# Kernel optimization log

Hardware: AMD Instinct MI355X
Metric: run time of the kernel (lower is better)

The kernel has to match this reference:

```python
import jax, jax.numpy as jnp
import numpy as np

B, C, H, W = 4, 512, 64, 64
HC = C // 2  # hidden_channel of Correlation


def setup_inputs() -> dict:
    key = jax.random.key(0)
    ks = jax.random.split(key, 7)
    s = 0.02
    return {
        "x": jax.random.normal(ks[0], (B, C, H, W), dtype=jnp.float32),
        "Wf": jax.random.normal(ks[1], (HC, C), dtype=jnp.float32) * s,
        "bf": jnp.zeros((HC,), dtype=jnp.float32),
        "Wg": jax.random.normal(ks[2], (HC, C), dtype=jnp.float32) * s,
        "bg": jnp.zeros((HC,), dtype=jnp.float32),
        "Wh": jax.random.normal(ks[3], (C, C), dtype=jnp.float32) * s,
        "bh": jnp.zeros((C,), dtype=jnp.float32),
    }


def reference(x, Wf, bf, Wg, bg, Wh, bh):
    b, c, h, w = x.shape
    n = h * w
    xf = x.reshape(b, c, n)  # hw_flatten: [B, C, N]
    # 1x1 convs == per-pixel linear projections
    f = jnp.einsum('oc,bcn->bon', Wf, xf) + bf[None, :, None]  # [B, HC, N]
    g = jnp.einsum('oc,bcn->bon', Wg, xf) + bg[None, :, None]  # [B, HC, N]
    hproj = jnp.einsum('oc,bcn->bon', Wh, xf) + bh[None, :, None]  # [B, C, N]
    # energy = f^T g : [B, N, N]
    energy = jnp.einsum('bcn,bcm->bnm', f, g)
    correlation = jax.nn.softmax(energy, axis=-1)
    # attention = mean over query axis n of correlation -> [B, 1, N]
    attention = jnp.mean(correlation, axis=1, keepdims=True)
    # residual = h @ correlation^T : sum_k h[b,c,k] * corr[b,j,k]
    residual = jnp.einsum('bck,bjk->bcj', hproj, correlation)
    residual = residual.reshape(b, c, h, w)
    attention = attention.reshape(b, 1, h, w)
    return residual, attention
```

## Files before the change

### kernel.cpp

```cpp
#include <hip/hip_runtime.h>
#include <cmath>

#define BATCH 4
#define CH    512
#define HCH   256
#define NPIX  4096
#define L2E   1.44269504088896340736f

typedef __attribute__((ext_vector_type(8))) short bf16x8;
typedef __attribute__((ext_vector_type(4))) float f32x4;

#define MFMA16(a, b, c) __builtin_amdgcn_mfma_f32_16x16x32_bf16((a), (b), (c), 0, 0, 0)

__device__ __forceinline__ unsigned short f2bf(float f) {
    unsigned int u = __float_as_uint(f);
    return (unsigned short)((u + 0x7fffu + ((u >> 16) & 1u)) >> 16);
}
__device__ __forceinline__ ushort4 pack4(float a, float b, float c, float d) {
    ushort4 u; u.x = f2bf(a); u.y = f2bf(b); u.z = f2bf(c); u.w = f2bf(d); return u;
}
__device__ __forceinline__ void gload16(const unsigned short* g, unsigned short* l) {
    __builtin_amdgcn_global_load_lds(
        (const __attribute__((address_space(1))) unsigned int*)g,
        (__attribute__((address_space(3))) unsigned int*)l, 16, 0, 0);
}

__global__ __launch_bounds__(256) void convert_w_kernel(
    const float* __restrict__ Wf, const float* __restrict__ Wg,
    const float* __restrict__ Wh, unsigned short* __restrict__ Wc)
{
    const int idx = blockIdx.x * 256 + threadIdx.x;
    const int o  = idx >> 7;
    const int c4 = (idx & 127) * 4;
    const float* src = (o < HCH)     ? (Wf + (size_t)o * CH + c4)
                     : (o < 2 * HCH) ? (Wg + (size_t)(o - HCH) * CH + c4)
                                     : (Wh + (size_t)(o - 2 * HCH) * CH + c4);
    float4 v = *(const float4*)src;
    *(ushort4*)&Wc[(size_t)o * CH + c4] = pack4(v.x, v.y, v.z, v.w);
}

__global__ __launch_bounds__(256) void convert_x_kernel(
    const float* __restrict__ x, unsigned short* __restrict__ Xp)
{
    __shared__ unsigned short Lt[64][40];
    const int b  = blockIdx.z;
    const int cb = blockIdx.y;
    const int n0 = blockIdx.x * 64;
    const int t  = threadIdx.x;
    const int cr = t >> 4;
    const int f4 = t & 15;
    #pragma unroll
    for (int p = 0; p < 2; ++p) {
        const int c = p * 16 + cr;
        float4 v = *(const float4*)(x + ((size_t)b * CH + cb * 32 + c) * NPIX + n0 + f4 * 4);
        Lt[f4 * 4 + 0][c] = f2bf(v.x);
        Lt[f4 * 4 + 1][c] = f2bf(v.y);
        Lt[f4 * 4 + 2][c] = f2bf(v.z);
        Lt[f4 * 4 + 3][c] = f2bf(v.w);
    }
    __syncthreads();
    const int n  = t >> 2;
    const int ch = t & 3;
    uint4 u = *(const uint4*)&Lt[n][ch * 8];
    *(uint4*)&Xp[((size_t)b * 16 + cb) * (NPIX * 32) + (size_t)(n0 + n) * 32 + ch * 8] = u;
}

__global__ __launch_bounds__(256, 2) void proj_fg_kernel(
    const unsigned short* __restrict__ Wc, const unsigned short* __restrict__ Xp,
    const float* __restrict__ bf, const float* __restrict__ bg,
    unsigned short* __restrict__ F, unsigned short* __restrict__ G)
{
    const int b  = blockIdx.z;
    const int n0 = blockIdx.x * 128;
    const int o0 = blockIdx.y * 128;
    const int t  = threadIdx.x;
    const int wave = t >> 6, lane = t & 63, quad = lane >> 4, l16 = lane & 15;
    const int ow = o0 + wave * 32;

    f32x4 acc[2][8];
    #pragma unroll
    for (int ms = 0; ms < 2; ++ms)
        #pragma unroll
        for (int ns = 0; ns < 8; ++ns) acc[ms][ns] = (f32x4){0.f, 0.f, 0.f, 0.f};

    const unsigned short* xb = Xp + (size_t)b * 16 * (NPIX * 32);
    for (int st = 0; st < 16; ++st) {
        bf16x8 a0 = *(const bf16x8*)&Wc[(size_t)(ow + l16) * CH + st * 32 + quad * 8];
        bf16x8 a1 = *(const bf16x8*)&Wc[(size_t)(ow + 16 + l16) * CH + st * 32 + quad * 8];
        const unsigned short* xs = xb + (size_t)st * (NPIX * 32) + quad * 8;
        #pragma unroll
        for (int ns = 0; ns < 8; ++ns) {
            bf16x8 bb = *(const bf16x8*)(xs + (size_t)(n0 + ns * 16 + l16) * 32);
            acc[0][ns] = MFMA16(a0, bb, acc[0][ns]);
            acc[1][ns] = MFMA16(a1, bb, acc[1][ns]);
        }
    }

    const int orow = quad * 4;
    #pragma unroll
    for (int ms = 0; ms < 2; ++ms) {
        const int ob = ow + ms * 16 + orow;
        float bias[4];
        #pragma unroll
        for (int r = 0; r < 4; ++r)
            bias[r] = (o0 < HCH) ? bf[ob + r] : bg[ob + r - HCH];
        #pragma unroll
        for (int ns = 0; ns < 8; ++ns) {
            const int n = n0 + ns * 16 + l16;
            ushort4 u = pack4(acc[ms][ns][0] + bias[0], acc[ms][ns][1] + bias[1],
                              acc[ms][ns][2] + bias[2], acc[ms][ns][3] + bias[3]);
            if (o0 < HCH) {
                *(ushort4*)&F[((size_t)b * NPIX + n) * HCH + ob] = u;
            } else {
                const int og = ob - HCH;
                const int cb = og >> 5, co = og & 31;
                *(ushort4*)&G[((size_t)b * 8 + cb) * (NPIX * 32) + (size_t)n * 32 + co] = u;
            }
        }
    }
}

__global__ __launch_bounds__(256, 2) void proj_v_kernel(
    const unsigned short* __restrict__ Wc, const unsigned short* __restrict__ Xp,
    const float* __restrict__ bh, unsigned short* __restrict__ V)
{
    const int b  = blockIdx.z;
    const int c0 = blockIdx.x * 128;
    const int p0 = blockIdx.y * 128;
    const int t  = threadIdx.x;
    const int wave = t >> 6, lane = t & 63, quad = lane >> 4, l16 = lane & 15;
    const int pw = p0 + wave * 32;

    f32x4 acc[2][8];
    #pragma unroll
    for (int ms = 0; ms < 2; ++ms)
        #pragma unroll
        for (int ns = 0; ns < 8; ++ns) acc[ms][ns] = (f32x4){0.f, 0.f, 0.f, 0.f};

    const unsigned short* xb = Xp + (size_t)b * 16 * (NPIX * 32);
    for (int st = 0; st < 16; ++st) {
        const unsigned short* xs = xb + (size_t)st * (NPIX * 32) + quad * 8;
        bf16x8 a0 = *(const bf16x8*)(xs + (size_t)(pw + l16) * 32);
        bf16x8 a1 = *(const bf16x8*)(xs + (size_t)(pw + 16 + l16) * 32);
        #pragma unroll
        for (int ns = 0; ns < 8; ++ns) {
            bf16x8 bb = *(const bf16x8*)&Wc[(size_t)(2 * HCH + c0 + ns * 16 + l16) * CH + st * 32 + quad * 8];
            acc[0][ns] = MFMA16(a0, bb, acc[0][ns]);
            acc[1][ns] = MFMA16(a1, bb, acc[1][ns]);
        }
    }

    float biasv[8];
    #pragma unroll
    for (int ns = 0; ns < 8; ++ns) biasv[ns] = bh[c0 + ns * 16 + l16];

    const int kb = pw >> 5;
    const int ko0 = quad * 4;
    const int cx = (l16 & 7) << 3;
    #pragma unroll
    for (int ms = 0; ms < 2; ++ms) {
        #pragma unroll
        for (int ns = 0; ns < 8; ++ns) {
            const int c = c0 + ns * 16 + l16;
            ushort4 u = pack4(acc[ms][ns][0] + biasv[ns], acc[ms][ns][1] + biasv[ns],
                              acc[ms][ns][2] + biasv[ns], acc[ms][ns][3] + biasv[ns]);
            const int el = (c * 32 + ms * 16 + ko0) ^ cx;
            *(ushort4*)&V[((size_t)b * 128 + kb) * (CH * 32) + el] = u;
        }
    }
}

__global__ __launch_bounds__(512, 4) void score_kernel(
    const unsigned short* __restrict__ F, const unsigned short* __restrict__ G,
    unsigned short* __restrict__ P, float* __restrict__ rowl)
{
    const int blk = blockIdx.x;
    const int xcd = blk & 7;
    const int b   = xcd >> 1;
    const int kh  = xcd & 1;
    const int q0  = (blk >> 3) * 64;
    const int t    = threadIdx.x;
    const int wave = t >> 6, lane = t & 63, quad = lane >> 4, l16 = lane & 15;
    const int qh = wave >> 2, kw = wave & 3;

    bf16x8 af[2][8];
    #pragma unroll
    for (int qs = 0; qs < 2; ++qs)
        #pragma unroll
        for (int st = 0; st < 8; ++st)
            af[qs][st] = *(const bf16x8*)&F[((size_t)b * NPIX + q0 + qh * 32 + qs * 16 + l16) * HCH + st * 32 + quad * 8];

    float ls[2][4];
    #pragma unroll
    for (int qs = 0; qs < 2; ++qs)
        #pragma unroll
        for (int r = 0; r < 4; ++r) ls[qs][r] = 0.f;

    const unsigned short* Gb = G + (size_t)b * 8 * (NPIX * 32);
    unsigned short* Pb2 = P + (size_t)b * 128 * (NPIX * 32) + (size_t)(q0 + qh * 32) * 32;
    const int qx = (quad & 1) * 4;

    const int kbeg = kh * 2048, kend = kbeg + 2048;
    for (int k0 = kbeg; k0 < kend; k0 += 128) {
        const int kk = k0 + kw * 32;
        f32x4 s[2][2];
        #pragma unroll
        for (int qs = 0; qs < 2; ++qs)
            #pragma unroll
            for (int ks = 0; ks < 2; ++ks) s[qs][ks] = (f32x4){0.f, 0.f, 0.f, 0.f};
        #pragma unroll
        for (int st = 0; st < 8; ++st) {
            const unsigned short* gs = Gb + (size_t)st * (NPIX * 32) + quad * 8;
            bf16x8 b0 = *(const bf16x8*)(gs + (size_t)(kk + l16) * 32);
            bf16x8 b1 = *(const bf16x8*)(gs + (size_t)(kk + 16 + l16) * 32);
            s[0][0] = MFMA16(af[0][st], b0, s[0][0]);
            s[1][0] = MFMA16(af[1][st], b0, s[1][0]);
            s[0][1] = MFMA16(af[0][st], b1, s[0][1]);
            s[1][1] = MFMA16(af[1][st], b1, s[1][1]);
        }

        unsigned short* pw = Pb2 + (size_t)(kk >> 5) * (NPIX * 32);
        #pragma unroll
        for (int qs = 0; qs < 2; ++qs)
            #pragma unroll
            for (int ks = 0; ks < 2; ++ks)
                #pragma unroll
                for (int r = 0; r < 4; ++r) {
                    float e = exp2f(L2E * s[qs][ks][r]);
                    const int el = ((qs * 16 + quad * 4 + r) * 32 + ks * 16 + l16)
                                   ^ ((qx + r) << 3);
                    pw[el] = f2bf(e);
                    ls[qs][r] += e;
                }
    }

    #pragma unroll
    for (int d = 1; d < 16; d <<= 1)
        #pragma unroll
        for (int qs = 0; qs < 2; ++qs)
            #pragma unroll
            for (int r = 0; r < 4; ++r) ls[qs][r] += __shfl_xor(ls[qs][r], d, 64);

    if (l16 == 0) {
        #pragma unroll
        for (int qs = 0; qs < 2; ++qs)
            #pragma unroll
            for (int r = 0; r < 4; ++r)
                atomicAdd(&rowl[(size_t)b * NPIX + q0 + qh * 32 + qs * 16 + quad * 4 + r], ls[qs][r]);
    }
}

__global__ __launch_bounds__(512, 4) void pv_kernel(
    const unsigned short* __restrict__ P, const unsigned short* __restrict__ V,
    const float* __restrict__ rowl, float* __restrict__ outres)
{
    __shared__ unsigned short Pl[2][64 * 32];
    __shared__ unsigned short Vl[2][256 * 32];
    const int blk = blockIdx.x;
    const int xcd = blk & 7;
    const int b   = xcd >> 1;
    const int ch  = xcd & 1;
    const int q0  = (blk >> 3) * 64;
    const int t    = threadIdx.x;
    const int wave = t >> 6, lane = t & 63, quad = lane >> 4, l16 = lane & 15;
    const int qw = wave >> 2;
    const int cw = wave & 3;
    const int cbase = cw * 64;

    const unsigned short* Pg = P + ((size_t)b * 128 * NPIX + q0) * 32;
    const unsigned short* Vg = V + ((size_t)b * 128 * CH + ch * 256) * 32;

    const int fx  = (l16 & 7) << 4;
    const int pA0 = (((qw * 32      + l16) * 64) + quad * 16) ^ fx;
    const int pA1 = (((qw * 32 + 16 + l16) * 64) + quad * 16) ^ fx;
    const int vO0 = (((cbase +  0 + l16) * 64) + quad * 16) ^ fx;
    const int vO1 = (((cbase + 16 + l16) * 64) + quad * 16) ^ fx;
    const int vO2 = (((cbase + 32 + l16) * 64) + quad * 16) ^ fx;
    const int vO3 = (((cbase + 48 + l16) * 64) + quad * 16) ^ fx;

    f32x4 O[2][4];
    #pragma unroll
    for (int qs = 0; qs < 2; ++qs)
        #pragma unroll
        for (int ct = 0; ct < 4; ++ct) O[qs][ct] = (f32x4){0.f, 0.f, 0.f, 0.f};

    auto stage = [&](int bb, int kb) {
        const unsigned short* vg = Vg + (size_t)kb * (CH * 32) + wave * 1024;
        unsigned short* vl = &Vl[bb][wave * 1024];
        gload16(vg + lane * 8,       vl);
        gload16(vg + 512 + lane * 8, vl + 512);
        if (wave < 4) {
            const unsigned short* pg = Pg + (size_t)kb * (NPIX * 32) + wave * 512;
            gload16(pg + lane * 8, &Pl[bb][wave * 512]);
        }
    };

    stage(0, 0);
    __syncthreads();

    int buf = 0;
    for (int kb = 0; kb < 128; ++kb) {
        if (kb + 1 < 128) stage(buf ^ 1, kb + 1);

        const char* pb = (const char*)&Pl[buf][0];
        const char* vb = (const char*)&Vl[buf][0];
        bf16x8 a0 = *(const bf16x8*)(pb + pA0);
        bf16x8 a1 = *(const bf16x8*)(pb + pA1);
        bf16x8 v0 = *(const bf16x8*)(vb + vO0);
        bf16x8 v1 = *(const bf16x8*)(vb + vO1);
        bf16x8 v2 = *(const bf16x8*)(vb + vO2);
        bf16x8 v3 = *(const bf16x8*)(vb + vO3);
        O[0][0] = MFMA16(a0, v0, O[0][0]);
        O[1][0] = MFMA16(a1, v0, O[1][0]);
        O[0][1] = MFMA16(a0, v1, O[0][1]);
        O[1][1] = MFMA16(a1, v1, O[1][1]);
        O[0][2] = MFMA16(a0, v2, O[0][2]);
        O[1][2] = MFMA16(a1, v2, O[1][2]);
        O[0][3] = MFMA16(a0, v3, O[0][3]);
        O[1][3] = MFMA16(a1, v3, O[1][3]);

        __syncthreads();
        buf ^= 1;
    }

    float lr[2][4];
    #pragma unroll
    for (int qs = 0; qs < 2; ++qs)
        #pragma unroll
        for (int r = 0; r < 4; ++r)
            lr[qs][r] = 1.0f / rowl[(size_t)b * NPIX + q0 + qw * 32 + qs * 16 + quad * 4 + r];

    const int cb2 = ch * 256 + cbase;
    #pragma unroll
    for (int qs = 0; qs < 2; ++qs) {
        #pragma unroll
        for (int ct = 0; ct < 4; ++ct) {
            f32x4 o = O[qs][ct];
            o[0] *= lr[qs][0]; o[1] *= lr[qs][1]; o[2] *= lr[qs][2]; o[3] *= lr[qs][3];
            const int c = cb2 + ct * 16 + l16;
            *(f32x4*)&outres[((size_t)b * CH + c) * NPIX + q0 + qw * 32 + qs * 16 + quad * 4] = o;
        }
    }
}

__global__ __launch_bounds__(256) void colsum_kernel(
    const unsigned short* __restrict__ P, const float* __restrict__ rowl,
    float* __restrict__ attnacc)
{
    __shared__ float CS[16][32];
    const int blk = blockIdx.x;
    const int b  = blk >> 7;
    const int kb = blk & 127;
    const int t  = threadIdx.x;
    const int ko2 = t & 15;
    const int qr  = t >> 4;
    const unsigned short* Pb = P + (size_t)(b * 128 + kb) * (NPIX * 32);
    const float* rl = rowl + (size_t)b * NPIX;
    const int qx = (qr & 7) << 3;

    float a0 = 0.f, a1 = 0.f;
    for (int q = qr; q < NPIX; q += 16) {
        unsigned int u = *(const unsigned int*)(Pb + ((q * 32 + ko2 * 2) ^ qx));
        float li = 1.0f / rl[q];
        a0 += __uint_as_float(u << 16) * li;
        a1 += __uint_as_float(u & 0xFFFF0000u) * li;
    }
    CS[qr][ko2 * 2]     = a0;
    CS[qr][ko2 * 2 + 1] = a1;
    __syncthreads();
    if (t < 32) {
        float s = 0.f;
        #pragma unroll
        for (int i = 0; i < 16; ++i) s += CS[i][t];
        attnacc[(size_t)b * NPIX + kb * 32 + t] = s;
    }
}

__global__ __launch_bounds__(512, 4) void stats_kernel(
    const unsigned short* __restrict__ F, const unsigned short* __restrict__ G,
    float* __restrict__ rowl)
{
    const int blk = blockIdx.x;
    const int xcd = blk & 7;
    const int b   = xcd >> 1;
    const int kh  = xcd & 1;
    const int q0  = (blk >> 3) * 64;
    const int t    = threadIdx.x;
    const int wave = t >> 6, lane = t & 63, quad = lane >> 4, l16 = lane & 15;
    const int qh = wave >> 2, kw = wave & 3;

    bf16x8 af[2][8];
    #pragma unroll
    for (int qs = 0; qs < 2; ++qs)
        #pragma unroll
        for (int st = 0; st < 8; ++st)
            af[qs][st] = *(const bf16x8*)&F[((size_t)b * NPIX + q0 + qh * 32 + qs * 16 + l16) * HCH + st * 32 + quad * 8];

    float ls[2][4];
    #pragma unroll
    for (int qs = 0; qs < 2; ++qs)
        #pragma unroll
        for (int r = 0; r < 4; ++r) ls[qs][r] = 0.f;

    const unsigned short* Gb = G + (size_t)b * 8 * (NPIX * 32);
    const int kbeg = kh * 2048, kend = kbeg + 2048;
    for (int k0 = kbeg; k0 < kend; k0 += 128) {
        const int kk = k0 + kw * 32;
        f32x4 s[2][2];
        #pragma unroll
        for (int qs = 0; qs < 2; ++qs)
            #pragma unroll
            for (int ks = 0; ks < 2; ++ks) s[qs][ks] = (f32x4){0.f, 0.f, 0.f, 0.f};
        #pragma unroll
        for (int st = 0; st < 8; ++st) {
            const unsigned short* gs = Gb + (size_t)st * (NPIX * 32) + quad * 8;
            bf16x8 b0 = *(const bf16x8*)(gs + (size_t)(kk + l16) * 32);
            bf16x8 b1 = *(const bf16x8*)(gs + (size_t)(kk + 16 + l16) * 32);
            s[0][0] = MFMA16(af[0][st], b0, s[0][0]);
            s[1][0] = MFMA16(af[1][st], b0, s[1][0]);
            s[0][1] = MFMA16(af[0][st], b1, s[0][1]);
            s[1][1] = MFMA16(af[1][st], b1, s[1][1]);
        }
        #pragma unroll
        for (int qs = 0; qs < 2; ++qs)
            #pragma unroll
            for (int r = 0; r < 4; ++r)
                ls[qs][r] += exp2f(L2E * s[qs][0][r]) + exp2f(L2E * s[qs][1][r]);
    }

    #pragma unroll
    for (int d = 1; d < 16; d <<= 1)
        #pragma unroll
        for (int qs = 0; qs < 2; ++qs)
            #pragma unroll
            for (int r = 0; r < 4; ++r) ls[qs][r] += __shfl_xor(ls[qs][r], d, 64);

    if (l16 == 0) {
        #pragma unroll
        for (int qs = 0; qs < 2; ++qs)
            #pragma unroll
            for (int r = 0; r < 4; ++r)
                atomicAdd(&rowl[(size_t)b * NPIX + q0 + qh * 32 + qs * 16 + quad * 4 + r], ls[qs][r]);
    }
}

__global__ __launch_bounds__(512, 4) void apply_kernel(
    const unsigned short* __restrict__ F, const unsigned short* __restrict__ G,
    const unsigned short* __restrict__ V, const float* __restrict__ rowl,
    float* __restrict__ outres, float* __restrict__ attnacc)
{
    __shared__ unsigned short Pl[2][32][136];
    const int blk = blockIdx.x;
    const int xcd = blk & 7;
    const int b   = xcd >> 1;
    const int ch  = xcd & 1;
    const int q0  = (blk >> 3) * 32;
    const int t    = threadIdx.x;
    const int wave = t >> 6, lane = t & 63, quad = lane >> 4, l16 = lane & 15;
    const int cw = ch * 256 + wave * 32;
    const int vx = (l16 & 7) << 3;

    float linv[2][4];
    #pragma unroll
    for (int qs = 0; qs < 2; ++qs)
        #pragma unroll
        for (int r = 0; r < 4; ++r)
            linv[qs][r] = 1.0f / rowl[(size_t)b * NPIX + q0 + qs * 16 + quad * 4 + r];

    f32x4 O[2][2];
    #pragma unroll
    for (int qs = 0; qs < 2; ++qs)
        #pragma unroll
        for (int ct = 0; ct < 2; ++ct) O[qs][ct] = (f32x4){0.f, 0.f, 0.f, 0.f};

    const unsigned short* Gb = G + (size_t)b * 8 * (NPIX * 32);
    const unsigned short* Vb = V + (size_t)b * 128 * (CH * 32);
    const unsigned short* Fq = F + ((size_t)b * NPIX + q0) * HCH;

    int buf = 0;
    for (int k0 = 0; k0 < NPIX; k0 += 128) {
        const int kk = k0 + wave * 16;
        f32x4 s[2];
        s[0] = (f32x4){0.f, 0.f, 0.f, 0.f};
        s[1] = (f32x4){0.f, 0.f, 0.f, 0.f};
        #pragma unroll
        for (int st = 0; st < 8; ++st) {
            bf16x8 a0 = *(const bf16x8*)&Fq[(size_t)l16 * HCH + st * 32 + quad * 8];
            bf16x8 a1 = *(const bf16x8*)&Fq[(size_t)(16 + l16) * HCH + st * 32 + quad * 8];
            bf16x8 bg = *(const bf16x8*)(Gb + (size_t)st * (NPIX * 32) + (size_t)(kk + l16) * 32 + quad * 8);
            s[0] = MFMA16(a0, bg, s[0]);
            s[1] = MFMA16(a1, bg, s[1]);
        }

        float p[2][4];
        #pragma unroll
        for (int qs = 0; qs < 2; ++qs)
            #pragma unroll
            for (int r = 0; r < 4; ++r)
                p[qs][r] = exp2f(L2E * s[qs][r]) * linv[qs][r];

        #pragma unroll
        for (int qs = 0; qs < 2; ++qs)
            #pragma unroll
            for (int r = 0; r < 4; ++r)
                Pl[buf][qs * 16 + quad * 4 + r][wave * 16 + l16] = f2bf(p[qs][r]);

        if (ch == 0) {
            float cs = p[0][0] + p[0][1] + p[0][2] + p[0][3]
                     + p[1][0] + p[1][1] + p[1][2] + p[1][3];
            cs += __shfl_xor(cs, 16, 64);
            cs += __shfl_xor(cs, 32, 64);
            if (quad == 0)
                atomicAdd(&attnacc[(size_t)b * NPIX + kk + l16], cs);
        }

        __syncthreads();

        #pragma unroll
        for (int ks = 0; ks < 4; ++ks) {
            bf16x8 pa0 = *(const bf16x8*)&Pl[buf][l16][ks * 32 + quad * 8];
            bf16x8 pa1 = *(const bf16x8*)&Pl[buf][16 + l16][ks * 32 + quad * 8];
            const unsigned short* vs = Vb + ((size_t)(k0 >> 5) + ks) * (CH * 32);
            #pragma unroll
            for (int ct = 0; ct < 2; ++ct) {
                const int el = (((cw + ct * 16 + l16) * 32) + quad * 8) ^ vx;
                bf16x8 vv = *(const bf16x8*)(vs + el);
                O[0][ct] = MFMA16(pa0, vv, O[0][ct]);
                O[1][ct] = MFMA16(pa1, vv, O[1][ct]);
            }
        }
        buf ^= 1;
    }

    #pragma unroll
    for (int qs = 0; qs < 2; ++qs) {
        #pragma unroll
        for (int ct = 0; ct < 2; ++ct) {
            const int c = cw + ct * 16 + l16;
            *(f32x4*)&outres[((size_t)b * CH + c) * NPIX + q0 + qs * 16 + quad * 4] = O[qs][ct];
        }
    }
}

__global__ __launch_bounds__(256) void attn_fin_kernel(
    const float* __restrict__ acc, float* __restrict__ outa)
{
    const int i = blockIdx.x * 256 + threadIdx.x;
    if (i < BATCH * NPIX) outa[i] = acc[i] * (1.0f / (float)NPIX);
}

extern "C" void kernel_launch(void* const* d_in, const int* in_sizes, int n_in,
                              void* d_out, int out_size, void* d_ws, size_t ws_size,
                              hipStream_t stream)
{
    (void)in_sizes; (void)n_in; (void)out_size;
    const float* x  = (const float*)d_in[0];
    const float* Wf = (const float*)d_in[1];
    const float* bf = (const float*)d_in[2];
    const float* Wg = (const float*)d_in[3];
    const float* bg = (const float*)d_in[4];
    const float* Wh = (const float*)d_in[5];
    const float* bh = (const float*)d_in[6];
    float* out = (float*)d_out;

    const size_t P_ELEMS  = (size_t)BATCH * 128 * NPIX * 32;
    const size_t XP_ELEMS = (size_t)BATCH * 16 * NPIX * 32;
    const size_t F_ELEMS  = (size_t)BATCH * NPIX * HCH;
    const size_t V_ELEMS  = (size_t)BATCH * 128 * CH * 32;
    const size_t NEED = (P_ELEMS + 2 * F_ELEMS + V_ELEMS) * 2
                      + (size_t)2 * BATCH * NPIX * 4;

    if (ws_size >= NEED) {
        unsigned short* P  = (unsigned short*)d_ws;
        unsigned short* Xp = P;
        unsigned short* Wc = P + XP_ELEMS;
        unsigned short* F  = P + P_ELEMS;
        unsigned short* G  = F + F_ELEMS;
        unsigned short* V  = G + F_ELEMS;
        float* rowl    = (float*)(V + V_ELEMS);
        float* attnacc = rowl + (size_t)BATCH * NPIX;

        hipMemsetAsync(rowl, 0, (size_t)BATCH * NPIX * sizeof(float), stream);

        convert_w_kernel<<<512, 256, 0, stream>>>(Wf, Wg, Wh, Wc);
        convert_x_kernel<<<dim3(NPIX / 64, 16, BATCH), 256, 0, stream>>>(x, Xp);

        proj_fg_kernel<<<dim3(NPIX / 128, 4, BATCH), 256, 0, stream>>>(Wc, Xp, bf, bg, F, G);
        proj_v_kernel<<<dim3(4, NPIX / 128, BATCH), 256, 0, stream>>>(Wc, Xp, bh, V);

        score_kernel<<<512, 512, 0, stream>>>(F, G, P, rowl);
        pv_kernel<<<512, 512, 0, stream>>>(P, V, rowl, out);
        colsum_kernel<<<512, 256, 0, stream>>>(P, rowl, attnacc);

        attn_fin_kernel<<<BATCH * NPIX / 256, 256, 0, stream>>>(
            attnacc, out + (size_t)BATCH * CH * NPIX);
    } else {
        unsigned short* Xp = (unsigned short*)d_ws;
        unsigned short* Wc = Xp + XP_ELEMS;
        unsigned short* F  = Wc + (size_t)1024 * CH;
        unsigned short* G  = F + F_ELEMS;
        unsigned short* V  = G + F_ELEMS;
        float* rowl    = (float*)(V + V_ELEMS);
        float* attnacc = rowl + (size_t)BATCH * NPIX;

        hipMemsetAsync(rowl, 0, (size_t)2 * BATCH * NPIX * sizeof(float), stream);

        convert_w_kernel<<<512, 256, 0, stream>>>(Wf, Wg, Wh, Wc);
        convert_x_kernel<<<dim3(NPIX / 64, 16, BATCH), 256, 0, stream>>>(x, Xp);

        proj_fg_kernel<<<dim3(NPIX / 128, 4, BATCH), 256, 0, stream>>>(Wc, Xp, bf, bg, F, G);
        proj_v_kernel<<<dim3(4, NPIX / 128, BATCH), 256, 0, stream>>>(Wc, Xp, bh, V);

        stats_kernel<<<512, 512, 0, stream>>>(F, G, rowl);
        apply_kernel<<<1024, 512, 0, stream>>>(F, G, V, rowl, out, attnacc);

        attn_fin_kernel<<<BATCH * NPIX / 256, 256, 0, stream>>>(
            attnacc, out + (size_t)BATCH * CH * NPIX);
    }
}
```

Measured before the change: 463.1 us.

## Stage swizzled G tiles in LDS via async loads in score kernel; shrink projection tiles

The score kernel now double-buffers 64-key tiles of G into shared memory with global_load_lds, replacing per-wave global loads of G. G is stored with an XOR swizzle so LDS reads avoid bank conflicts, and the stats and apply kernels read it through the same swizzle. The projection kernels use half-width tiles with a higher occupancy bound, which gives more blocks for parallelism. The cost is added block-wide barriers in every k iteration, and each wave now computes a smaller key slice per step.

```diff
diff --git a/kernel.cpp b/kernel.cpp
--- a/kernel.cpp
+++ b/kernel.cpp
@@ -65,23 +65,23 @@
     *(uint4*)&Xp[((size_t)b * 16 + cb) * (NPIX * 32) + (size_t)(n0 + n) * 32 + ch * 8] = u;
 }
 
-__global__ __launch_bounds__(256, 2) void proj_fg_kernel(
+__global__ __launch_bounds__(256, 4) void proj_fg_kernel(
     const unsigned short* __restrict__ Wc, const unsigned short* __restrict__ Xp,
     const float* __restrict__ bf, const float* __restrict__ bg,
     unsigned short* __restrict__ F, unsigned short* __restrict__ G)
 {
     const int b  = blockIdx.z;
-    const int n0 = blockIdx.x * 128;
+    const int n0 = blockIdx.x * 64;
     const int o0 = blockIdx.y * 128;
     const int t  = threadIdx.x;
     const int wave = t >> 6, lane = t & 63, quad = lane >> 4, l16 = lane & 15;
     const int ow = o0 + wave * 32;
 
-    f32x4 acc[2][8];
+    f32x4 acc[2][4];
     #pragma unroll
     for (int ms = 0; ms < 2; ++ms)
         #pragma unroll
-        for (int ns = 0; ns < 8; ++ns) acc[ms][ns] = (f32x4){0.f, 0.f, 0.f, 0.f};
+        for (int ns = 0; ns < 4; ++ns) acc[ms][ns] = (f32x4){0.f, 0.f, 0.f, 0.f};
 
     const unsigned short* xb = Xp + (size_t)b * 16 * (NPIX * 32);
     for (int st = 0; st < 16; ++st) {
@@ -89,7 +89,7 @@
         bf16x8 a1 = *(const bf16x8*)&Wc[(size_t)(ow + 16 + l16) * CH + st * 32 + quad * 8];
         const unsigned short* xs = xb + (size_t)st * (NPIX * 32) + quad * 8;
         #pragma unroll
-        for (int ns = 0; ns < 8; ++ns) {
+        for (int ns = 0; ns < 4; ++ns) {
             bf16x8 bb = *(const bf16x8*)(xs + (size_t)(n0 + ns * 16 + l16) * 32);
             acc[0][ns] = MFMA16(a0, bb, acc[0][ns]);
             acc[1][ns] = MFMA16(a1, bb, acc[1][ns]);
@@ -97,6 +97,7 @@
     }
 
     const int orow = quad * 4;
+    const int gx = (l16 & 7) << 3;
     #pragma unroll
     for (int ms = 0; ms < 2; ++ms) {
         const int ob = ow + ms * 16 + orow;
@@ -105,7 +106,7 @@
         for (int r = 0; r < 4; ++r)
             bias[r] = (o0 < HCH) ? bf[ob + r] : bg[ob + r - HCH];
         #pragma unroll
-        for (int ns = 0; ns < 8; ++ns) {
+        for (int ns = 0; ns < 4; ++ns) {
             const int n = n0 + ns * 16 + l16;
             ushort4 u = pack4(acc[ms][ns][0] + bias[0], acc[ms][ns][1] + bias[1],
                               acc[ms][ns][2] + bias[2], acc[ms][ns][3] + bias[3]);
@@ -114,28 +115,29 @@
             } else {
                 const int og = ob - HCH;
                 const int cb = og >> 5, co = og & 31;
-                *(ushort4*)&G[((size_t)b * 8 + cb) * (NPIX * 32) + (size_t)n * 32 + co] = u;
+                const int el = (n * 32 + co) ^ gx;
+                *(ushort4*)&G[((size_t)b * 8 + cb) * (NPIX * 32) + el] = u;
             }
         }
     }
 }
 
-__global__ __launch_bounds__(256, 2) void proj_v_kernel(
+__global__ __launch_bounds__(256, 4) void proj_v_kernel(
     const unsigned short* __restrict__ Wc, const unsigned short* __restrict__ Xp,
     const float* __restrict__ bh, unsigned short* __restrict__ V)
 {
     const int b  = blockIdx.z;
-    const int c0 = blockIdx.x * 128;
+    const int c0 = blockIdx.x * 64;
     const int p0 = blockIdx.y * 128;
     const int t  = threadIdx.x;
     const int wave = t >> 6, lane = t & 63, quad = lane >> 4, l16 = lane & 15;
     const int pw = p0 + wave * 32;
 
-    f32x4 acc[2][8];
+    f32x4 acc[2][4];
     #pragma unroll
     for (int ms = 0; ms < 2; ++ms)
         #pragma unroll
-        for (int ns = 0; ns < 8; ++ns) acc[ms][ns] = (f32x4){0.f, 0.f, 0.f, 0.f};
+        for (int ns = 0; ns < 4; ++ns) acc[ms][ns] = (f32x4){0.f, 0.f, 0.f, 0.f};
 
     const unsigned short* xb = Xp + (size_t)b * 16 * (NPIX * 32);
     for (int st = 0; st < 16; ++st) {
@@ -143,16 +145,16 @@
         bf16x8 a0 = *(const bf16x8*)(xs + (size_t)(pw + l16) * 32);
         bf16x8 a1 = *(const bf16x8*)(xs + (size_t)(pw + 16 + l16) * 32);
         #pragma unroll
-        for (int ns = 0; ns < 8; ++ns) {
+        for (int ns = 0; ns < 4; ++ns) {
             bf16x8 bb = *(const bf16x8*)&Wc[(size_t)(2 * HCH + c0 + ns * 16 + l16) * CH + st * 32 + quad * 8];
             acc[0][ns] = MFMA16(a0, bb, acc[0][ns]);
             acc[1][ns] = MFMA16(a1, bb, acc[1][ns]);
         }
     }
 
-    float biasv[8];
-    #pragma unroll
-    for (int ns = 0; ns < 8; ++ns) biasv[ns] = bh[c0 + ns * 16 + l16];
+    float biasv[4];
+    #pragma unroll
+    for (int ns = 0; ns < 4; ++ns) biasv[ns] = bh[c0 + ns * 16 + l16];
 
     const int kb = pw >> 5;
     const int ko0 = quad * 4;
@@ -160,7 +162,7 @@
     #pragma unroll
     for (int ms = 0; ms < 2; ++ms) {
         #pragma unroll
-        for (int ns = 0; ns < 8; ++ns) {
+        for (int ns = 0; ns < 4; ++ns) {
             const int c = c0 + ns * 16 + l16;
             ushort4 u = pack4(acc[ms][ns][0] + biasv[ns], acc[ms][ns][1] + biasv[ns],
                               acc[ms][ns][2] + biasv[ns], acc[ms][ns][3] + biasv[ns]);
@@ -174,6 +176,7 @@
     const unsigned short* __restrict__ F, const unsigned short* __restrict__ G,
     unsigned short* __restrict__ P, float* __restrict__ rowl)
 {
+    __shared__ unsigned short Gl[2][8 * 64 * 32];
     const int blk = blockIdx.x;
     const int xcd = blk & 7;
     const int b   = xcd >> 1;
@@ -200,38 +203,57 @@
     unsigned short* Pb2 = P + (size_t)b * 128 * (NPIX * 32) + (size_t)(q0 + qh * 32) * 32;
     const int qx = (quad & 1) * 4;
 
-    const int kbeg = kh * 2048, kend = kbeg + 2048;
-    for (int k0 = kbeg; k0 < kend; k0 += 128) {
-        const int kk = k0 + kw * 32;
-        f32x4 s[2][2];
-        #pragma unroll
-        for (int qs = 0; qs < 2; ++qs)
-            #pragma unroll
-            for (int ks = 0; ks < 2; ++ks) s[qs][ks] = (f32x4){0.f, 0.f, 0.f, 0.f};
+    const int kbeg = kh * 2048;
+
+    auto stage = [&](int bb, int kt) {
+        const size_t kofs = (size_t)(kbeg + kt * 64) * 32;
+        #pragma unroll
+        for (int j = 0; j < 4; ++j) {
+            const int cbse = j * 512 + wave * 64;
+            const int cb   = cbse >> 8;
+            const int o16  = cbse & 255;
+            const unsigned short* g = Gb + (size_t)cb * (NPIX * 32) + kofs
+                                        + o16 * 8 + lane * 8;
+            gload16(g, &Gl[bb][cb * 2048 + o16 * 8]);
+        }
+    };
+
+    const int fx = (l16 & 7) << 4;
+    const int bO = (((kw * 16 + l16) * 64) + quad * 16) ^ fx;
+
+    stage(0, 0);
+    __syncthreads();
+
+    int buf = 0;
+    for (int kt = 0; kt < 32; ++kt) {
+        if (kt + 1 < 32) stage(buf ^ 1, kt + 1);
+
+        f32x4 s[2];
+        s[0] = (f32x4){0.f, 0.f, 0.f, 0.f};
+        s[1] = (f32x4){0.f, 0.f, 0.f, 0.f};
+        const char* gb = (const char*)&Gl[buf][0];
         #pragma unroll
         for (int st = 0; st < 8; ++st) {
-            const unsigned short* gs = Gb + (size_t)st * (NPIX * 32) + quad * 8;
-            bf16x8 b0 = *(const bf16x8*)(gs + (size_t)(kk + l16) * 32);
-            bf16x8 b1 = *(const bf16x8*)(gs + (size_t)(kk + 16 + l16) * 32);
-            s[0][0] = MFMA16(af[0][st], b0, s[0][0]);
-            s[1][0] = MFMA16(af[1][st], b0, s[1][0]);
-            s[0][1] = MFMA16(af[0][st], b1, s[0][1]);
-            s[1][1] = MFMA16(af[1][st], b1, s[1][1]);
-        }
-
-        unsigned short* pw = Pb2 + (size_t)(kk >> 5) * (NPIX * 32);
-        #pragma unroll
-        for (int qs = 0; qs < 2; ++qs)
-            #pragma unroll
-            for (int ks = 0; ks < 2; ++ks)
-                #pragma unroll
-                for (int r = 0; r < 4; ++r) {
-                    float e = exp2f(L2E * s[qs][ks][r]);
-                    const int el = ((qs * 16 + quad * 4 + r) * 32 + ks * 16 + l16)
-                                   ^ ((qx + r) << 3);
-                    pw[el] = f2bf(e);
-                    ls[qs][r] += e;
-                }
+            bf16x8 bb = *(const bf16x8*)(gb + st * 4096 + bO);
+            s[0] = MFMA16(af[0][st], bb, s[0]);
+            s[1] = MFMA16(af[1][st], bb, s[1]);
+        }
+
+        const int kkk = kbeg + kt * 64 + kw * 16;
+        unsigned short* pw = Pb2 + (size_t)(kkk >> 5) * (NPIX * 32);
+        const int kcol = (kw & 1) * 16 + l16;
+        #pragma unroll
+        for (int qs = 0; qs < 2; ++qs)
+            #pragma unroll
+            for (int r = 0; r < 4; ++r) {
+                float e = exp2f(L2E * s[qs][r]);
+                const int el = ((qs * 16 + quad * 4 + r) * 32 + kcol) ^ ((qx + r) << 3);
+                pw[el] = f2bf(e);
+                ls[qs][r] += e;
+            }
+
+        __syncthreads();
+        buf ^= 1;
     }
 
     #pragma unroll
@@ -388,6 +410,7 @@
     const int t    = threadIdx.x;
     const int wave = t >> 6, lane = t & 63, quad = lane >> 4, l16 = lane & 15;
     const int qh = wave >> 2, kw = wave & 3;
+    const int gx = (l16 & 7) << 3;
 
     bf16x8 af[2][8];
     #pragma unroll
@@ -413,9 +436,9 @@
             for (int ks = 0; ks < 2; ++ks) s[qs][ks] = (f32x4){0.f, 0.f, 0.f, 0.f};
         #pragma unroll
         for (int st = 0; st < 8; ++st) {
-            const unsigned short* gs = Gb + (size_t)st * (NPIX * 32) + quad * 8;
-            bf16x8 b0 = *(const bf16x8*)(gs + (size_t)(kk + l16) * 32);
-            bf16x8 b1 = *(const bf16x8*)(gs + (size_t)(kk + 16 + l16) * 32);
+            const unsigned short* gs = Gb + (size_t)st * (NPIX * 32);
+            bf16x8 b0 = *(const bf16x8*)(gs + ((((kk + l16) * 32) + quad * 8) ^ gx));
+            bf16x8 b1 = *(const bf16x8*)(gs + ((((kk + 16 + l16) * 32) + quad * 8) ^ gx));
             s[0][0] = MFMA16(af[0][st], b0, s[0][0]);
             s[1][0] = MFMA16(af[1][st], b0, s[1][0]);
             s[0][1] = MFMA16(af[0][st], b1, s[0][1]);
@@ -459,6 +482,7 @@
     const int wave = t >> 6, lane = t & 63, quad = lane >> 4, l16 = lane & 15;
     const int cw = ch * 256 + wave * 32;
     const int vx = (l16 & 7) << 3;
+    const int gx = (l16 & 7) << 3;
 
     float linv[2][4];
     #pragma unroll
@@ -487,7 +511,8 @@
         for (int st = 0; st < 8; ++st) {
             bf16x8 a0 = *(const bf16x8*)&Fq[(size_t)l16 * HCH + st * 32 + quad * 8];
             bf16x8 a1 = *(const bf16x8*)&Fq[(size_t)(16 + l16) * HCH + st * 32 + quad * 8];
-            bf16x8 bg = *(const bf16x8*)(Gb + (size_t)st * (NPIX * 32) + (size_t)(kk + l16) * 32 + quad * 8);
+            bf16x8 bg = *(const bf16x8*)(Gb + (size_t)st * (NPIX * 32)
+                                         + ((((kk + l16) * 32) + quad * 8) ^ gx));
             s[0] = MFMA16(a0, bg, s[0]);
             s[1] = MFMA16(a1, bg, s[1]);
         }
@@ -585,8 +610,8 @@
         convert_w_kernel<<<512, 256, 0, stream>>>(Wf, Wg, Wh, Wc);
         convert_x_kernel<<<dim3(NPIX / 64, 16, BATCH), 256, 0, stream>>>(x, Xp);
 
-        proj_fg_kernel<<<dim3(NPIX / 128, 4, BATCH), 256, 0, stream>>>(Wc, Xp, bf, bg, F, G);
-        proj_v_kernel<<<dim3(4, NPIX / 128, BATCH), 256, 0, stream>>>(Wc, Xp, bh, V);
+        proj_fg_kernel<<<dim3(NPIX / 64, 4, BATCH), 256, 0, stream>>>(Wc, Xp, bf, bg, F, G);
+        proj_v_kernel<<<dim3(8, NPIX / 128, BATCH), 256, 0, stream>>>(Wc, Xp, bh, V);
 
         score_kernel<<<512, 512, 0, stream>>>(F, G, P, rowl);
         pv_kernel<<<512, 512, 0, stream>>>(P, V, rowl, out);
@@ -608,8 +633,8 @@
         convert_w_kernel<<<512, 256, 0, stream>>>(Wf, Wg, Wh, Wc);
         convert_x_kernel<<<dim3(NPIX / 64, 16, BATCH), 256, 0, stream>>>(x, Xp);
 
-        proj_fg_kernel<<<dim3(NPIX / 128, 4, BATCH), 256, 0, stream>>>(Wc, Xp, bf, bg, F, G);
-        proj_v_kernel<<<dim3(4, NPIX / 128, BATCH), 256, 0, stream>>>(Wc, Xp, bh, V);
+        proj_fg_kernel<<<dim3(NPIX / 64, 4, BATCH), 256, 0, stream>>>(Wc, Xp, bf, bg, F, G);
+        proj_v_kernel<<<dim3(8, NPIX / 128, BATCH), 256, 0, stream>>>(Wc, Xp, bh, V);
 
         stats_kernel<<<512, 512, 0, stream>>>(F, G, rowl);
         apply_kernel<<<1024, 512, 0, stream>>>(F, G, V, rowl, out, attnacc);
```

New measurement: 415.0 us. 1.12x faster.
